# Performance work log

Hardware: AMD Instinct MI355X
Metric: run time of the kernel (lower is better)

## Reference

```python
import jax, jax.numpy as jnp
import numpy as np

N_EMBD = 768
N_HEAD = 12
HEAD_DIM = N_EMBD // N_HEAD  # 64


def setup_inputs() -> dict:
    key = jax.random.key(0)
    k1, k2, k3 = jax.random.split(key, 3)
    B, S = 4, 2048
    x = jax.random.normal(k1, (B, S, N_EMBD), dtype=jnp.float32)
    W_attn = jax.random.normal(k2, (N_EMBD, 3 * N_EMBD), dtype=jnp.float32) * 0.02
    b_attn = jax.random.normal(k3, (3 * N_EMBD,), dtype=jnp.float32) * 0.02
    return {"x": x, "W_attn": W_attn, "b_attn": b_attn}


def reference(x, W_attn, b_attn):
    B, S, E = x.shape
    H, D = N_HEAD, HEAD_DIM
    # fused QKV projection (torch Linear: x @ W^T + b; here W_attn stored as [E, 3E])
    qkv = x @ W_attn + b_attn  # [B, S, 3E]
    q, k, v = jnp.split(qkv, 3, axis=-1)
    q = q.reshape(B, S, H, D)
    k = k.reshape(B, S, H, D)
    v = v.reshape(B, S, H, D)
    scale = 1.0 / np.sqrt(D).astype(np.float32)
    scores = jnp.einsum('bqhd,bkhd->bhqk', q, k) * scale  # [B, H, S, S]
    causal = jnp.tril(jnp.ones((S, S), dtype=bool))
    # ReLU attention nonlinearity (no softmax); masked entries -> 0
    att = jnp.where(causal, jnp.maximum(scores, 0.0), 0.0)
    y = jnp.einsum('bhqk,bkhd->bqhd', att, v)  # [B, S, H, D]
    return y.reshape(B, S, E)
```

## Files before the change

### kernel.cpp

```cpp
#include <hip/hip_runtime.h>

typedef __attribute__((ext_vector_type(8))) short short8;
typedef __attribute__((ext_vector_type(4))) float floatx4;
typedef __attribute__((ext_vector_type(4))) unsigned int uint4v;

#define S_LEN 2048
#define NH 12
#define HD 64
#define EMB 768
#define E3 2304

#define MF(a, b, c) __builtin_amdgcn_mfma_f32_16x16x32_bf16(a, b, c, 0, 0, 0)

__device__ __forceinline__ unsigned short f2bf(float f) {
    unsigned int u = __builtin_bit_cast(unsigned int, f);
    u += 0x7FFFu + ((u >> 16) & 1u);
    return (unsigned short)(u >> 16);
}

__device__ __forceinline__ unsigned int pack2bf(float a, float b) {
#if __has_builtin(__builtin_amdgcn_cvt_pk_bf16_f32)
    typedef __attribute__((ext_vector_type(2))) short short2v;
    short2v r = __builtin_amdgcn_cvt_pk_bf16_f32(a, b);
    return __builtin_bit_cast(unsigned int, r);
#else
    return (unsigned int)f2bf(a) | ((unsigned int)f2bf(b) << 16);
#endif
}

__device__ __forceinline__ void pl32_swap(unsigned int& x, unsigned int& y) {
#if __has_builtin(__builtin_amdgcn_permlane32_swap)
    typedef __attribute__((ext_vector_type(2))) unsigned int uint2v_;
    uint2v_ r = __builtin_amdgcn_permlane32_swap(x, y, false, false);
    x = r[0]; y = r[1];
#else
    asm("v_permlane32_swap_b32 %0, %1" : "+v"(x), "+v"(y));
#endif
}
__device__ __forceinline__ void pl16_swap(unsigned int& x, unsigned int& y) {
#if __has_builtin(__builtin_amdgcn_permlane16_swap)
    typedef __attribute__((ext_vector_type(2))) unsigned int uint2v_;
    uint2v_ r = __builtin_amdgcn_permlane16_swap(x, y, false, false);
    x = r[0]; y = r[1];
#else
    asm("v_permlane16_swap_b32 %0, %1" : "+v"(x), "+v"(y));
#endif
}

__device__ __forceinline__ void gl_lds16(const void* g, void* l) {
    __builtin_amdgcn_global_load_lds(
        (const __attribute__((address_space(1))) unsigned int*)g,
        (__attribute__((address_space(3))) unsigned int*)l, 16, 0, 0);
}

__global__ __launch_bounds__(256) void conv_fused(const float* __restrict__ x,
                                                  ushort* __restrict__ xb,
                                                  const float* __restrict__ W,
                                                  ushort* __restrict__ Wt) {
    int tid = threadIdx.x;
    if (blockIdx.x < 6144) {
        int i = (blockIdx.x * 256 + tid) * 4;
        float4 f = *(const float4*)(x + i);
        ushort4 o;
        o.x = f2bf(f.x); o.y = f2bf(f.y); o.z = f2bf(f.z); o.w = f2bf(f.w);
        *(ushort4*)(xb + i) = o;
    } else {
        __shared__ float tile[32][33];
        int b2 = blockIdx.x - 6144;
        int n0 = (b2 % 72) * 32, k0 = (b2 / 72) * 32;
        int tx = tid & 31, ty = tid >> 5;
        for (int i = 0; i < 4; i++)
            tile[ty + i * 8][tx] = W[(size_t)(k0 + ty + i * 8) * E3 + n0 + tx];
        __syncthreads();
        for (int i = 0; i < 4; i++)
            Wt[(size_t)(n0 + ty + i * 8) * EMB + k0 + tx] = f2bf(tile[tx][ty + i * 8]);
    }
}

__global__ __launch_bounds__(512, 1) void qkv_gemm(const ushort* __restrict__ Xb,
                                                   const ushort* __restrict__ Wt,
                                                   const float* __restrict__ bias,
                                                   ushort* __restrict__ QKb,
                                                   ushort* __restrict__ Vt) {
    extern __shared__ char ldsb[];
    const int tid  = threadIdx.x;
    const int w = tid >> 6, lane = tid & 63;
    const int l15 = lane & 15, quad = lane >> 4;
    const int r8 = lane >> 3, cc = lane & 7;
    const int wm = w >> 1, wn = w & 1;
    const int m0 = blockIdx.x * 256, n0 = blockIdx.y * 128;

    floatx4 acc[4][4] = {};

    const char* agp = (const char*)Xb + (size_t)(m0 + w * 32 + r8) * 1536 + (cc ^ r8) * 16;
    const char* bgp = (const char*)Wt + (size_t)(n0 + w * 16 + r8) * 1536 + (cc ^ r8) * 16;
    const int adstB = w * 4096;
    const int bdstB = 32768 + w * 2048;

    const int aroB = (wm * 64 + l15) * 128;
    const int broB = 32768 + (wn * 64 + l15) * 128;
    const int swz0 = ((quad) ^ (l15 & 7)) * 16;
    const int swz1 = ((4 + quad) ^ (l15 & 7)) * 16;

    for (int i = 0; i < 4; i++) gl_lds16(agp + i * 12288, ldsb + adstB + i * 1024);
    for (int i = 0; i < 2; i++) gl_lds16(bgp + i * 12288, ldsb + bdstB + i * 1024);
    for (int i = 0; i < 4; i++) gl_lds16(agp + 128 + i * 12288, ldsb + 49152 + adstB + i * 1024);
    for (int i = 0; i < 2; i++) gl_lds16(bgp + 128 + i * 12288, ldsb + 49152 + bdstB + i * 1024);

#pragma unroll
    for (int t = 0; t < 12; ++t) {
        if (t < 11) asm volatile("s_waitcnt vmcnt(6)" ::: "memory");
        else        asm volatile("s_waitcnt vmcnt(0)" ::: "memory");
        __builtin_amdgcn_s_barrier();
        __builtin_amdgcn_sched_barrier(0);

        const char* base = ldsb + (t % 3) * 49152;
        char* sdst = ldsb + ((t + 2) % 3) * 49152;
        const int koff = (t + 2) * 128;
        const bool st = (t < 10);

        short8 af0, af1, bf0, bf1, bf2, bf3;

        af0 = *(const short8*)(base + aroB + 0 * 2048 + swz0);
        af1 = *(const short8*)(base + aroB + 1 * 2048 + swz0);
        bf0 = *(const short8*)(base + broB + 0 * 2048 + swz0);
        bf1 = *(const short8*)(base + broB + 1 * 2048 + swz0);
        bf2 = *(const short8*)(base + broB + 2 * 2048 + swz0);
        bf3 = *(const short8*)(base + broB + 3 * 2048 + swz0);
        if (st) { gl_lds16(agp + koff,         sdst + adstB);
                  gl_lds16(agp + koff + 12288, sdst + adstB + 1024); }
        __builtin_amdgcn_s_setprio(1);
        acc[0][0] = MF(af0, bf0, acc[0][0]); acc[0][1] = MF(af0, bf1, acc[0][1]);
        acc[0][2] = MF(af0, bf2, acc[0][2]); acc[0][3] = MF(af0, bf3, acc[0][3]);
        acc[1][0] = MF(af1, bf0, acc[1][0]); acc[1][1] = MF(af1, bf1, acc[1][1]);
        acc[1][2] = MF(af1, bf2, acc[1][2]); acc[1][3] = MF(af1, bf3, acc[1][3]);
        __builtin_amdgcn_s_setprio(0);
        __builtin_amdgcn_s_barrier();

        af0 = *(const short8*)(base + aroB + 2 * 2048 + swz0);
        af1 = *(const short8*)(base + aroB + 3 * 2048 + swz0);
        if (st) { gl_lds16(agp + koff + 2 * 12288, sdst + adstB + 2048);
                  gl_lds16(agp + koff + 3 * 12288, sdst + adstB + 3072); }
        __builtin_amdgcn_s_setprio(1);
        acc[2][0] = MF(af0, bf0, acc[2][0]); acc[2][1] = MF(af0, bf1, acc[2][1]);
        acc[2][2] = MF(af0, bf2, acc[2][2]); acc[2][3] = MF(af0, bf3, acc[2][3]);
        acc[3][0] = MF(af1, bf0, acc[3][0]); acc[3][1] = MF(af1, bf1, acc[3][1]);
        acc[3][2] = MF(af1, bf2, acc[3][2]); acc[3][3] = MF(af1, bf3, acc[3][3]);
        __builtin_amdgcn_s_setprio(0);
        __builtin_amdgcn_s_barrier();

        af0 = *(const short8*)(base + aroB + 0 * 2048 + swz1);
        af1 = *(const short8*)(base + aroB + 1 * 2048 + swz1);
        bf0 = *(const short8*)(base + broB + 0 * 2048 + swz1);
        bf1 = *(const short8*)(base + broB + 1 * 2048 + swz1);
        bf2 = *(const short8*)(base + broB + 2 * 2048 + swz1);
        bf3 = *(const short8*)(base + broB + 3 * 2048 + swz1);
        if (st) { gl_lds16(bgp + koff,         sdst + bdstB);
                  gl_lds16(bgp + koff + 12288, sdst + bdstB + 1024); }
        __builtin_amdgcn_s_setprio(1);
        acc[0][0] = MF(af0, bf0, acc[0][0]); acc[0][1] = MF(af0, bf1, acc[0][1]);
        acc[0][2] = MF(af0, bf2, acc[0][2]); acc[0][3] = MF(af0, bf3, acc[0][3]);
        acc[1][0] = MF(af1, bf0, acc[1][0]); acc[1][1] = MF(af1, bf1, acc[1][1]);
        acc[1][2] = MF(af1, bf2, acc[1][2]); acc[1][3] = MF(af1, bf3, acc[1][3]);
        __builtin_amdgcn_s_setprio(0);
        __builtin_amdgcn_s_barrier();

        af0 = *(const short8*)(base + aroB + 2 * 2048 + swz1);
        af1 = *(const short8*)(base + aroB + 3 * 2048 + swz1);
        __builtin_amdgcn_s_setprio(1);
        acc[2][0] = MF(af0, bf0, acc[2][0]); acc[2][1] = MF(af0, bf1, acc[2][1]);
        acc[2][2] = MF(af0, bf2, acc[2][2]); acc[2][3] = MF(af0, bf3, acc[2][3]);
        acc[3][0] = MF(af1, bf0, acc[3][0]); acc[3][1] = MF(af1, bf1, acc[3][1]);
        acc[3][2] = MF(af1, bf2, acc[3][2]); acc[3][3] = MF(af1, bf3, acc[3][3]);
        __builtin_amdgcn_s_setprio(0);
    }

    __syncthreads();
    ushort* epi = (ushort*)ldsb;
    int seg = n0 >= 1536 ? 2 : (n0 >= 768 ? 1 : 0);
    if (seg < 2) {
        float scale = (seg == 0) ? 0.125f : 1.0f;
        for (int ni = 0; ni < 4; ni++) {
            int nl = wn * 64 + ni * 16 + l15;
            float bv = bias[n0 + nl];
            for (int mi = 0; mi < 4; mi++)
                for (int r = 0; r < 4; r++) {
                    int ml = wm * 64 + mi * 16 + quad * 4 + r;
                    epi[ml * 132 + nl] = f2bf((acc[mi][ni][r] + bv) * scale);
                }
        }
        __syncthreads();
        int row = tid >> 1, h2 = tid & 1;
        size_t gm = (size_t)(m0 + row);
        for (int i = 0; i < 8; i++) {
            uint4 v = *(const uint4*)&epi[row * 132 + h2 * 64 + i * 8];
            *(uint4*)&QKb[gm * 1536 + n0 + h2 * 64 + i * 8] = v;
        }
    } else {
        for (int ni = 0; ni < 4; ni++) {
            int nl = wn * 64 + ni * 16 + l15;
            float bv = bias[n0 + nl];
            for (int mi = 0; mi < 4; mi++) {
                int ml = wm * 64 + mi * 16 + quad * 4;
                ushort4 p4;
                p4.x = f2bf(acc[mi][ni][0] + bv);
                p4.y = f2bf(acc[mi][ni][1] + bv);
                p4.z = f2bf(acc[mi][ni][2] + bv);
                p4.w = f2bf(acc[mi][ni][3] + bv);
                *(ushort4*)&epi[nl * 264 + ml] = p4;
            }
        }
        __syncthreads();
        int row = tid >> 2, q4 = tid & 3;
        int nn = n0 + row - 1536;
        int hh = nn >> 6, d = nn & 63;
        int bb = m0 >> 11, s0 = m0 & 2047;
        for (int i = 0; i < 8; i++) {
            uint4 v = *(const uint4*)&epi[row * 264 + q4 * 64 + i * 8];
            *(uint4*)&Vt[((size_t)(bb * NH + hh) * HD + d) * S_LEN + s0 + q4 * 64 + i * 8] = v;
        }
    }
}

__global__ __launch_bounds__(256) void attn(const ushort* __restrict__ QKb,
                                            const ushort* __restrict__ Vt,
                                            float* __restrict__ out) {
    __shared__ ushort lds[32768];
    char* ldsb = (char*)lds;
    int tid = threadIdx.x;
    int w = tid >> 6, lane = tid & 63;
    int l15 = lane & 15, quad = lane >> 4;
    int r8 = lane >> 3, cc = lane & 7;
    int rr = lane >> 4;

    int kfo[2];
    for (int ch = 0; ch < 2; ch++)
        kfo[ch] = l15 * 128 + ((ch * 4 + quad) ^ (l15 & 7)) * 16;
    int vfo2[4];
    for (int T = 0; T < 4; T++)
        vfo2[T] = 32768 + l15 * 256 + ((T * 4 + quad) ^ l15) * 16;
    int rhs[2] = { w * 32 + l15, w * 32 + 16 + l15 };
    int kgo = (w * 32 + r8) * 3072 + (cc ^ r8) * 16;
    int vgo[4];
    for (int i = 0; i < 4; i++)
        vgo[i] = (w * 16 + i * 4 + rr) * 4096 + (((lane & 15) ^ ((i * 4 + rr) & 15)) * 16);
    int kst = (w * 32) * 128;
    int vst = 32768 + (w * 16) * 256;

    int b = blockIdx.x;
    int nit, qts[2], bhs[2];
    if (b < 240)      { nit = 1; qts[0] = 15 - b / 48; bhs[0] = b % 48; qts[1] = 0; bhs[1] = 0; }
    else if (b < 480) { int j = b - 240; nit = 2; qts[0] = 10 - j / 48; bhs[0] = j % 48;
                        qts[1] = 1 + j / 48; bhs[1] = j % 48; }
    else              { int j = b - 480; nit = 2; qts[0] = 0; bhs[0] = 2 * j;
                        qts[1] = 0; bhs[1] = 2 * j + 1; }

    const char* kg[2]; const char* vg[2];
    for (int i = 0; i < 2; i++) {
        int bh = bhs[i], bg = bh / NH, h = bh % NH;
        kg[i] = (const char*)(QKb + (size_t)bg * S_LEN * 1536 + 768 + h * 64) + kgo;
        vg[i] = (const char*)(Vt + (size_t)bh * HD * S_LEN);
    }

    auto prefetch = [&](const char* kbase, const char* vbase, int dstP) {
        for (int i = 0; i < 4; i++)
            gl_lds16(kbase + i * 24576, ldsb + dstP * 16384 + kst + i * 1024);
        for (int i = 0; i < 4; i++)
            gl_lds16(vbase + vgo[i], ldsb + dstP * 16384 + vst + i * 1024);
    };

    int p = 0;
    prefetch(kg[0], vg[0], 0);
    for (int ii = 0; ii < nit; ii++) {
        int qt = qts[ii];
        int bh = bhs[ii], bg = bh / NH, h = bh % NH;
        const ushort* Qcol = QKb + (size_t)bg * S_LEN * 1536 + h * 64;
        short8 qf[2][2];
        for (int nq = 0; nq < 2; nq++)
            for (int ch = 0; ch < 2; ch++)
                qf[nq][ch] = *(const short8*)(Qcol +
                    (size_t)(qt * 128 + w * 32 + nq * 16 + l15) * 1536 + ch * 32 + quad * 8);

        floatx4 acco[2][4] = {};
        int nst = qt + 1;
        for (int st = 0; st < nst; st++) {
            __syncthreads();
            if (st + 1 < nst)
                prefetch(kg[ii] + (size_t)(st + 1) * 393216, vg[ii] + (st + 1) * 256, p ^ 1);
            else if (ii + 1 < nit)
                prefetch(kg[ii + 1], vg[ii + 1], p ^ 1);

            bool diag = (st == qt);
            const char* kb = ldsb + p * 16384;

            for (int jsub = 0; jsub < 2; jsub++) {
                floatx4 stc[4][2] = {};
                for (int ch = 0; ch < 2; ch++) {
                    short8 kf[4];
                    for (int mk = 0; mk < 4; mk++)
                        kf[mk] = *(const short8*)(kb + kfo[ch] + jsub * 8192 + mk * 2048);
                    for (int mk = 0; mk < 4; mk++)
                        for (int nq = 0; nq < 2; nq++)
                            stc[mk][nq] = __builtin_amdgcn_mfma_f32_16x16x32_bf16(
                                kf[mk], qf[nq][ch], stc[mk][nq], 0, 0, 0);
                }

                unsigned int pk[4][2][2];
                for (int mk = 0; mk < 4; mk++) {
                    for (int nq = 0; nq < 2; nq++) {
                        float e[4];
                        for (int r = 0; r < 4; r++)
                            e[r] = fmaxf(stc[mk][nq][r], 0.0f);
                        if (diag) {
                            int kl = jsub * 64 + mk * 16 + quad * 4;
                            for (int r = 0; r < 4; r++)
                                if (kl + r > rhs[nq]) e[r] = 0.0f;
                        }
                        pk[mk][nq][0] = pack2bf(e[0], e[1]);
                        pk[mk][nq][1] = pack2bf(e[2], e[3]);
                    }
                }

                for (int pr = 0; pr < 2; pr++) {
                    int T = jsub * 2 + pr;
                    short8 vf[4];
                    for (int ni = 0; ni < 4; ni++)
                        vf[ni] = *(const short8*)(kb + vfo2[T] + ni * 4096);
                    for (int mi = 0; mi < 2; mi++) {
                        unsigned int a0 = pk[2 * pr][mi][0], a1 = pk[2 * pr][mi][1];
                        unsigned int b0 = pk[2 * pr + 1][mi][0], b1 = pk[2 * pr + 1][mi][1];
                        pl32_swap(a0, b0);  pl32_swap(a1, b1);
                        pl16_swap(a0, b0);  pl16_swap(a1, b1);
                        short8 af = __builtin_bit_cast(short8, (uint4v){a0, a1, b0, b1});
                        for (int ni = 0; ni < 4; ni++)
                            acco[mi][ni] = __builtin_amdgcn_mfma_f32_16x16x32_bf16(
                                af, vf[ni], acco[mi][ni], 0, 0, 0);
                    }
                }
            }
            p ^= 1;
        }

        for (int mi = 0; mi < 2; mi++) {
            for (int ni = 0; ni < 4; ni++) {
                int d = ni * 16 + l15;
                for (int r = 0; r < 4; r++) {
                    int s = qt * 128 + w * 32 + mi * 16 + quad * 4 + r;
                    out[((size_t)bg * S_LEN + s) * EMB + h * 64 + d] = acco[mi][ni][r];
                }
            }
        }
    }
}

extern "C" void kernel_launch(void* const* d_in, const int* in_sizes, int n_in,
                              void* d_out, int out_size, void* d_ws, size_t ws_size,
                              hipStream_t stream) {
    const float* x    = (const float*)d_in[0];
    const float* W    = (const float*)d_in[1];
    const float* bias = (const float*)d_in[2];
    float* out = (float*)d_out;

    char* ws = (char*)d_ws;
    const size_t SZ_X  = (size_t)8192 * EMB * 2;
    const size_t SZ_W  = (size_t)E3 * EMB * 2;
    const size_t SZ_QK = (size_t)8192 * 1536 * 2;
    ushort* Xb  = (ushort*)(ws);
    ushort* Wt  = (ushort*)(ws + SZ_X);
    ushort* QKb = (ushort*)(ws + SZ_X + SZ_W);
    ushort* Vt  = (ushort*)(ws + SZ_X + SZ_W + SZ_QK);

    static bool attr_done = false;
    if (!attr_done) {
        hipFuncSetAttribute((const void*)qkv_gemm,
                            hipFuncAttributeMaxDynamicSharedMemorySize, 147456);
        attr_done = true;
    }

    conv_fused<<<dim3(6144 + 1728), dim3(256), 0, stream>>>(x, Xb, W, Wt);
    qkv_gemm<<<dim3(32, 18), dim3(512), 147456, stream>>>(Xb, Wt, bias, QKb, Vt);
    attn<<<dim3(504), dim3(256), 0, stream>>>(QKb, Vt, out);
}
```

Measured before the change: 186.5 us.

## Load V fragments directly from global, halve LDS, add occupancy and diagonal skip

V tiles are no longer staged through LDS. Each wave reads its V fragments straight from global memory into registers, which halves LDS use per block and lets launch_bounds request two blocks per CU. The change also staggers the jsub order across waves, skips the fully masked upper sub-block on the diagonal tile for the first two waves, and raises wave priority around the MFMA sections. The cost is uncoalesced global V loads whose latency is no longer hidden by async prefetch, along with tighter register pressure at the higher occupancy.

```diff
diff --git a/kernel.cpp b/kernel.cpp
--- a/kernel.cpp
+++ b/kernel.cpp
@@ -222,30 +222,23 @@
     }
 }
 
-__global__ __launch_bounds__(256) void attn(const ushort* __restrict__ QKb,
-                                            const ushort* __restrict__ Vt,
-                                            float* __restrict__ out) {
-    __shared__ ushort lds[32768];
+__global__ __launch_bounds__(256, 2) void attn(const ushort* __restrict__ QKb,
+                                               const ushort* __restrict__ Vt,
+                                               float* __restrict__ out) {
+    __shared__ ushort lds[16384];
     char* ldsb = (char*)lds;
     int tid = threadIdx.x;
     int w = tid >> 6, lane = tid & 63;
     int l15 = lane & 15, quad = lane >> 4;
     int r8 = lane >> 3, cc = lane & 7;
-    int rr = lane >> 4;
 
     int kfo[2];
     for (int ch = 0; ch < 2; ch++)
         kfo[ch] = l15 * 128 + ((ch * 4 + quad) ^ (l15 & 7)) * 16;
-    int vfo2[4];
-    for (int T = 0; T < 4; T++)
-        vfo2[T] = 32768 + l15 * 256 + ((T * 4 + quad) ^ l15) * 16;
     int rhs[2] = { w * 32 + l15, w * 32 + 16 + l15 };
     int kgo = (w * 32 + r8) * 3072 + (cc ^ r8) * 16;
-    int vgo[4];
-    for (int i = 0; i < 4; i++)
-        vgo[i] = (w * 16 + i * 4 + rr) * 4096 + (((lane & 15) ^ ((i * 4 + rr) & 15)) * 16);
     int kst = (w * 32) * 128;
-    int vst = 32768 + (w * 16) * 256;
+    const int vlo = l15 * S_LEN + quad * 8;
 
     int b = blockIdx.x;
     int nit, qts[2], bhs[2];
@@ -255,22 +248,20 @@
     else              { int j = b - 480; nit = 2; qts[0] = 0; bhs[0] = 2 * j;
                         qts[1] = 0; bhs[1] = 2 * j + 1; }
 
-    const char* kg[2]; const char* vg[2];
+    const char* kg[2]; const ushort* vb[2];
     for (int i = 0; i < 2; i++) {
         int bh = bhs[i], bg = bh / NH, h = bh % NH;
         kg[i] = (const char*)(QKb + (size_t)bg * S_LEN * 1536 + 768 + h * 64) + kgo;
-        vg[i] = (const char*)(Vt + (size_t)bh * HD * S_LEN);
-    }
-
-    auto prefetch = [&](const char* kbase, const char* vbase, int dstP) {
+        vb[i] = Vt + (size_t)bh * HD * S_LEN;
+    }
+
+    auto prefK = [&](const char* kbase, int dstP) {
         for (int i = 0; i < 4; i++)
             gl_lds16(kbase + i * 24576, ldsb + dstP * 16384 + kst + i * 1024);
-        for (int i = 0; i < 4; i++)
-            gl_lds16(vbase + vgo[i], ldsb + dstP * 16384 + vst + i * 1024);
     };
 
     int p = 0;
-    prefetch(kg[0], vg[0], 0);
+    prefK(kg[0], 0);
     for (int ii = 0; ii < nit; ii++) {
         int qt = qts[ii];
         int bh = bhs[ii], bg = bh / NH, h = bh % NH;
@@ -280,21 +271,34 @@
             for (int ch = 0; ch < 2; ch++)
                 qf[nq][ch] = *(const short8*)(Qcol +
                     (size_t)(qt * 128 + w * 32 + nq * 16 + l15) * 1536 + ch * 32 + quad * 8);
+        const ushort* vp[4];
+        for (int ni = 0; ni < 4; ni++)
+            vp[ni] = vb[ii] + (size_t)ni * 16 * S_LEN + vlo;
 
         floatx4 acco[2][4] = {};
         int nst = qt + 1;
         for (int st = 0; st < nst; st++) {
             __syncthreads();
             if (st + 1 < nst)
-                prefetch(kg[ii] + (size_t)(st + 1) * 393216, vg[ii] + (st + 1) * 256, p ^ 1);
+                prefK(kg[ii] + (size_t)(st + 1) * 393216, p ^ 1);
             else if (ii + 1 < nit)
-                prefetch(kg[ii + 1], vg[ii + 1], p ^ 1);
+                prefK(kg[ii + 1], p ^ 1);
 
             bool diag = (st == qt);
             const char* kb = ldsb + p * 16384;
-
-            for (int jsub = 0; jsub < 2; jsub++) {
+            int k0 = st * 128;
+
+            for (int js = 0; js < 2; js++) {
+                int jsub = js ^ (w & 1);
+                if (diag && w < 2 && jsub == 1) continue;
+
+                short8 vf[2][4];
+                for (int t2 = 0; t2 < 2; t2++)
+                    for (int ni = 0; ni < 4; ni++)
+                        vf[t2][ni] = *(const short8*)(vp[ni] + k0 + jsub * 64 + t2 * 32);
+
                 floatx4 stc[4][2] = {};
+                __builtin_amdgcn_s_setprio(1);
                 for (int ch = 0; ch < 2; ch++) {
                     short8 kf[4];
                     for (int mk = 0; mk < 4; mk++)
@@ -304,6 +308,7 @@
                             stc[mk][nq] = __builtin_amdgcn_mfma_f32_16x16x32_bf16(
                                 kf[mk], qf[nq][ch], stc[mk][nq], 0, 0, 0);
                 }
+                __builtin_amdgcn_s_setprio(0);
 
                 unsigned int pk[4][2][2];
                 for (int mk = 0; mk < 4; mk++) {
@@ -321,11 +326,8 @@
                     }
                 }
 
+                __builtin_amdgcn_s_setprio(1);
                 for (int pr = 0; pr < 2; pr++) {
-                    int T = jsub * 2 + pr;
-                    short8 vf[4];
-                    for (int ni = 0; ni < 4; ni++)
-                        vf[ni] = *(const short8*)(kb + vfo2[T] + ni * 4096);
                     for (int mi = 0; mi < 2; mi++) {
                         unsigned int a0 = pk[2 * pr][mi][0], a1 = pk[2 * pr][mi][1];
                         unsigned int b0 = pk[2 * pr + 1][mi][0], b1 = pk[2 * pr + 1][mi][1];
@@ -334,9 +336,10 @@
                         short8 af = __builtin_bit_cast(short8, (uint4v){a0, a1, b0, b1});
                         for (int ni = 0; ni < 4; ni++)
                             acco[mi][ni] = __builtin_amdgcn_mfma_f32_16x16x32_bf16(
-                                af, vf[ni], acco[mi][ni], 0, 0, 0);
+                                af, vf[pr][ni], acco[mi][ni], 0, 0, 0);
                     }
                 }
+                __builtin_amdgcn_s_setprio(0);
             }
             p ^= 1;
         }
```

Result: slower. 196.8 us (+5.6%).

## Process two adjacent query tiles per block sharing K/V tile loads

Applied to the files above, without the earlier changes.

The attention kernel now assigns each block a pair of adjacent 128-row query tiles for one (batch, head). Each K/V tile is streamed into LDS once and reused by both query tiles, replacing the previous 504-block load-balancing schedule with 384 blocks. Load imbalance remains because the tile pairs have different causal lengths. The change also adds s_setprio around the MFMA sections and a launch_bounds occupancy hint of 2, at the cost of more accumulator registers.

```diff
diff --git a/kernel.cpp b/kernel.cpp
--- a/kernel.cpp
+++ b/kernel.cpp
@@ -222,16 +222,15 @@
     }
 }
 
-__global__ __launch_bounds__(256) void attn(const ushort* __restrict__ QKb,
-                                            const ushort* __restrict__ Vt,
-                                            float* __restrict__ out) {
+__global__ __launch_bounds__(256, 2) void attn(const ushort* __restrict__ QKb,
+                                               const ushort* __restrict__ Vt,
+                                               float* __restrict__ out) {
     __shared__ ushort lds[32768];
     char* ldsb = (char*)lds;
     int tid = threadIdx.x;
     int w = tid >> 6, lane = tid & 63;
     int l15 = lane & 15, quad = lane >> 4;
     int r8 = lane >> 3, cc = lane & 7;
-    int rr = lane >> 4;
 
     int kfo[2];
     for (int ch = 0; ch < 2; ch++)
@@ -243,58 +242,60 @@
     int kgo = (w * 32 + r8) * 3072 + (cc ^ r8) * 16;
     int vgo[4];
     for (int i = 0; i < 4; i++)
-        vgo[i] = (w * 16 + i * 4 + rr) * 4096 + (((lane & 15) ^ ((i * 4 + rr) & 15)) * 16);
+        vgo[i] = (w * 16 + i * 4 + quad) * 4096 + ((l15 ^ ((i * 4 + quad) & 15)) * 16);
     int kst = (w * 32) * 128;
     int vst = 32768 + (w * 16) * 256;
 
     int b = blockIdx.x;
-    int nit, qts[2], bhs[2];
-    if (b < 240)      { nit = 1; qts[0] = 15 - b / 48; bhs[0] = b % 48; qts[1] = 0; bhs[1] = 0; }
-    else if (b < 480) { int j = b - 240; nit = 2; qts[0] = 10 - j / 48; bhs[0] = j % 48;
-                        qts[1] = 1 + j / 48; bhs[1] = j % 48; }
-    else              { int j = b - 480; nit = 2; qts[0] = 0; bhs[0] = 2 * j;
-                        qts[1] = 0; bhs[1] = 2 * j + 1; }
-
-    const char* kg[2]; const char* vg[2];
-    for (int i = 0; i < 2; i++) {
-        int bh = bhs[i], bg = bh / NH, h = bh % NH;
-        kg[i] = (const char*)(QKb + (size_t)bg * S_LEN * 1536 + 768 + h * 64) + kgo;
-        vg[i] = (const char*)(Vt + (size_t)bh * HD * S_LEN);
-    }
-
-    auto prefetch = [&](const char* kbase, const char* vbase, int dstP) {
+    int j = 7 - b / 48, bh = b % 48;
+    int qts2[2] = { 2 * j, 2 * j + 1 };
+    int bg = bh / NH, h = bh % NH;
+    const char* kg = (const char*)(QKb + (size_t)bg * S_LEN * 1536 + 768 + h * 64) + kgo;
+    const char* vgb = (const char*)(Vt + (size_t)bh * HD * S_LEN);
+
+    auto prefetch = [&](int st, int dstP) {
+        const char* kbase = kg + (size_t)st * 393216;
+        const char* vbase = vgb + st * 256;
         for (int i = 0; i < 4; i++)
             gl_lds16(kbase + i * 24576, ldsb + dstP * 16384 + kst + i * 1024);
         for (int i = 0; i < 4; i++)
             gl_lds16(vbase + vgo[i], ldsb + dstP * 16384 + vst + i * 1024);
     };
 
-    int p = 0;
-    prefetch(kg[0], vg[0], 0);
-    for (int ii = 0; ii < nit; ii++) {
-        int qt = qts[ii];
-        int bh = bhs[ii], bg = bh / NH, h = bh % NH;
-        const ushort* Qcol = QKb + (size_t)bg * S_LEN * 1536 + h * 64;
-        short8 qf[2][2];
+    const ushort* Qcol = QKb + (size_t)bg * S_LEN * 1536 + h * 64;
+    short8 qf[2][2][2];
+    for (int tq = 0; tq < 2; tq++)
         for (int nq = 0; nq < 2; nq++)
             for (int ch = 0; ch < 2; ch++)
-                qf[nq][ch] = *(const short8*)(Qcol +
-                    (size_t)(qt * 128 + w * 32 + nq * 16 + l15) * 1536 + ch * 32 + quad * 8);
-
-        floatx4 acco[2][4] = {};
-        int nst = qt + 1;
-        for (int st = 0; st < nst; st++) {
-            __syncthreads();
-            if (st + 1 < nst)
-                prefetch(kg[ii] + (size_t)(st + 1) * 393216, vg[ii] + (st + 1) * 256, p ^ 1);
-            else if (ii + 1 < nit)
-                prefetch(kg[ii + 1], vg[ii + 1], p ^ 1);
-
-            bool diag = (st == qt);
-            const char* kb = ldsb + p * 16384;
-
-            for (int jsub = 0; jsub < 2; jsub++) {
+                qf[tq][nq][ch] = *(const short8*)(Qcol +
+                    (size_t)(qts2[tq] * 128 + w * 32 + nq * 16 + l15) * 1536 + ch * 32 + quad * 8);
+
+    floatx4 acco[2][2][4] = {};
+    int nst = qts2[1] + 1;
+    int p = 0;
+    prefetch(0, 0);
+    for (int st = 0; st < nst; st++) {
+        __syncthreads();
+        if (st + 1 < nst) prefetch(st + 1, p ^ 1);
+
+        const char* kb = ldsb + p * 16384;
+
+#pragma unroll
+        for (int jsub = 0; jsub < 2; jsub++) {
+            short8 vf[2][4];
+            for (int pr = 0; pr < 2; pr++) {
+                int T = jsub * 2 + pr;
+                for (int ni = 0; ni < 4; ni++)
+                    vf[pr][ni] = *(const short8*)(kb + vfo2[T] + ni * 4096);
+            }
+
+#pragma unroll
+            for (int tq = 0; tq < 2; tq++) {
+                if (st > qts2[tq]) continue;
+                bool diag = (st == qts2[tq]);
+
                 floatx4 stc[4][2] = {};
+                __builtin_amdgcn_s_setprio(1);
                 for (int ch = 0; ch < 2; ch++) {
                     short8 kf[4];
                     for (int mk = 0; mk < 4; mk++)
@@ -302,8 +303,9 @@
                     for (int mk = 0; mk < 4; mk++)
                         for (int nq = 0; nq < 2; nq++)
                             stc[mk][nq] = __builtin_amdgcn_mfma_f32_16x16x32_bf16(
-                                kf[mk], qf[nq][ch], stc[mk][nq], 0, 0, 0);
-                }
+                                kf[mk], qf[tq][nq][ch], stc[mk][nq], 0, 0, 0);
+                }
+                __builtin_amdgcn_s_setprio(0);
 
                 unsigned int pk[4][2][2];
                 for (int mk = 0; mk < 4; mk++) {
@@ -321,11 +323,8 @@
                     }
                 }
 
+                __builtin_amdgcn_s_setprio(1);
                 for (int pr = 0; pr < 2; pr++) {
-                    int T = jsub * 2 + pr;
-                    short8 vf[4];
-                    for (int ni = 0; ni < 4; ni++)
-                        vf[ni] = *(const short8*)(kb + vfo2[T] + ni * 4096);
                     for (int mi = 0; mi < 2; mi++) {
                         unsigned int a0 = pk[2 * pr][mi][0], a1 = pk[2 * pr][mi][1];
                         unsigned int b0 = pk[2 * pr + 1][mi][0], b1 = pk[2 * pr + 1][mi][1];
@@ -333,20 +332,23 @@
                         pl16_swap(a0, b0);  pl16_swap(a1, b1);
                         short8 af = __builtin_bit_cast(short8, (uint4v){a0, a1, b0, b1});
                         for (int ni = 0; ni < 4; ni++)
-                            acco[mi][ni] = __builtin_amdgcn_mfma_f32_16x16x32_bf16(
-                                af, vf[ni], acco[mi][ni], 0, 0, 0);
+                            acco[tq][mi][ni] = __builtin_amdgcn_mfma_f32_16x16x32_bf16(
+                                af, vf[pr][ni], acco[tq][mi][ni], 0, 0, 0);
                     }
                 }
+                __builtin_amdgcn_s_setprio(0);
             }
-            p ^= 1;
-        }
-
+        }
+        p ^= 1;
+    }
+
+    for (int tq = 0; tq < 2; tq++) {
         for (int mi = 0; mi < 2; mi++) {
             for (int ni = 0; ni < 4; ni++) {
                 int d = ni * 16 + l15;
                 for (int r = 0; r < 4; r++) {
-                    int s = qt * 128 + w * 32 + mi * 16 + quad * 4 + r;
-                    out[((size_t)bg * S_LEN + s) * EMB + h * 64 + d] = acco[mi][ni][r];
+                    int s = qts2[tq] * 128 + w * 32 + mi * 16 + quad * 4 + r;
+                    out[((size_t)bg * S_LEN + s) * EMB + h * 64 + d] = acco[tq][mi][ni][r];
                 }
             }
         }
@@ -379,5 +381,5 @@
 
     conv_fused<<<dim3(6144 + 1728), dim3(256), 0, stream>>>(x, Xb, W, Wt);
     qkv_gemm<<<dim3(32, 18), dim3(512), 147456, stream>>>(Xb, Wt, bias, QKb, Vt);
-    attn<<<dim3(504), dim3(256), 0, stream>>>(QKb, Vt, out);
-}
+    attn<<<dim3(384), dim3(256), 0, stream>>>(QKb, Vt, out);
+}
```

Measured after the change: 189.8 us. No clear change (+1.8%).

## Shrink attention tiles to 64 queries and 64 keys per block, drop paired scheduling

Applied to the files above, without the earlier changes.

The attention kernel now uses 128-thread blocks handling a 64-row query tile with 64-key stages, launching 1536 blocks ordered longest-first instead of 504 blocks that paired short and long tiles. LDS usage halves and launch bounds allow multiple blocks per CU, aiming at better load balance and occupancy across the causal triangle. The trade-off is that each K/V stage is reused by fewer queries, which means more global/LDS traffic per FLOP and more barriers per unit of work.

```diff
diff --git a/kernel.cpp b/kernel.cpp
--- a/kernel.cpp
+++ b/kernel.cpp
@@ -222,132 +222,115 @@
     }
 }
 
-__global__ __launch_bounds__(256) void attn(const ushort* __restrict__ QKb,
-                                            const ushort* __restrict__ Vt,
-                                            float* __restrict__ out) {
-    __shared__ ushort lds[32768];
+__global__ __launch_bounds__(128, 2) void attn(const ushort* __restrict__ QKb,
+                                               const ushort* __restrict__ Vt,
+                                               float* __restrict__ out) {
+    __shared__ ushort lds[16384];
     char* ldsb = (char*)lds;
     int tid = threadIdx.x;
     int w = tid >> 6, lane = tid & 63;
     int l15 = lane & 15, quad = lane >> 4;
     int r8 = lane >> 3, cc = lane & 7;
-    int rr = lane >> 4;
 
     int kfo[2];
     for (int ch = 0; ch < 2; ch++)
         kfo[ch] = l15 * 128 + ((ch * 4 + quad) ^ (l15 & 7)) * 16;
-    int vfo2[4];
-    for (int T = 0; T < 4; T++)
-        vfo2[T] = 32768 + l15 * 256 + ((T * 4 + quad) ^ l15) * 16;
+    int vfo[2];
+    for (int T = 0; T < 2; T++)
+        vfo[T] = 16384 + l15 * 128 + ((T * 4 + quad) ^ (l15 & 7)) * 16;
     int rhs[2] = { w * 32 + l15, w * 32 + 16 + l15 };
     int kgo = (w * 32 + r8) * 3072 + (cc ^ r8) * 16;
     int vgo[4];
     for (int i = 0; i < 4; i++)
-        vgo[i] = (w * 16 + i * 4 + rr) * 4096 + (((lane & 15) ^ ((i * 4 + rr) & 15)) * 16);
+        vgo[i] = (w * 32 + i * 8 + r8) * 4096 + (cc ^ r8) * 16;
     int kst = (w * 32) * 128;
-    int vst = 32768 + (w * 16) * 256;
+    int vst = 16384 + (w * 32) * 128;
 
     int b = blockIdx.x;
-    int nit, qts[2], bhs[2];
-    if (b < 240)      { nit = 1; qts[0] = 15 - b / 48; bhs[0] = b % 48; qts[1] = 0; bhs[1] = 0; }
-    else if (b < 480) { int j = b - 240; nit = 2; qts[0] = 10 - j / 48; bhs[0] = j % 48;
-                        qts[1] = 1 + j / 48; bhs[1] = j % 48; }
-    else              { int j = b - 480; nit = 2; qts[0] = 0; bhs[0] = 2 * j;
-                        qts[1] = 0; bhs[1] = 2 * j + 1; }
-
-    const char* kg[2]; const char* vg[2];
-    for (int i = 0; i < 2; i++) {
-        int bh = bhs[i], bg = bh / NH, h = bh % NH;
-        kg[i] = (const char*)(QKb + (size_t)bg * S_LEN * 1536 + 768 + h * 64) + kgo;
-        vg[i] = (const char*)(Vt + (size_t)bh * HD * S_LEN);
-    }
-
-    auto prefetch = [&](const char* kbase, const char* vbase, int dstP) {
+    int qs = 31 - b / 48, bh = b % 48;
+    int bg = bh / NH, h = bh % NH;
+
+    const char* kg = (const char*)(QKb + (size_t)bg * S_LEN * 1536 + 768 + h * 64) + kgo;
+    const char* vgb = (const char*)(Vt + (size_t)bh * HD * S_LEN);
+
+    auto prefetch = [&](int st, int dstP) {
+        const char* kbase = kg + (size_t)st * 196608;
+        const char* vbase = vgb + st * 128;
         for (int i = 0; i < 4; i++)
-            gl_lds16(kbase + i * 24576, ldsb + dstP * 16384 + kst + i * 1024);
+            gl_lds16(kbase + i * 24576, ldsb + dstP * 8192 + kst + i * 1024);
         for (int i = 0; i < 4; i++)
-            gl_lds16(vbase + vgo[i], ldsb + dstP * 16384 + vst + i * 1024);
+            gl_lds16(vbase + vgo[i], ldsb + dstP * 8192 + vst + i * 1024);
     };
 
+    const ushort* Qcol = QKb + (size_t)bg * S_LEN * 1536 + h * 64;
+    short8 qf[2][2];
+    for (int nq = 0; nq < 2; nq++)
+        for (int ch = 0; ch < 2; ch++)
+            qf[nq][ch] = *(const short8*)(Qcol +
+                (size_t)(qs * 64 + w * 32 + nq * 16 + l15) * 1536 + ch * 32 + quad * 8);
+
+    floatx4 acco[2][4] = {};
     int p = 0;
-    prefetch(kg[0], vg[0], 0);
-    for (int ii = 0; ii < nit; ii++) {
-        int qt = qts[ii];
-        int bh = bhs[ii], bg = bh / NH, h = bh % NH;
-        const ushort* Qcol = QKb + (size_t)bg * S_LEN * 1536 + h * 64;
-        short8 qf[2][2];
-        for (int nq = 0; nq < 2; nq++)
-            for (int ch = 0; ch < 2; ch++)
-                qf[nq][ch] = *(const short8*)(Qcol +
-                    (size_t)(qt * 128 + w * 32 + nq * 16 + l15) * 1536 + ch * 32 + quad * 8);
-
-        floatx4 acco[2][4] = {};
-        int nst = qt + 1;
-        for (int st = 0; st < nst; st++) {
-            __syncthreads();
-            if (st + 1 < nst)
-                prefetch(kg[ii] + (size_t)(st + 1) * 393216, vg[ii] + (st + 1) * 256, p ^ 1);
-            else if (ii + 1 < nit)
-                prefetch(kg[ii + 1], vg[ii + 1], p ^ 1);
-
-            bool diag = (st == qt);
-            const char* kb = ldsb + p * 16384;
-
-            for (int jsub = 0; jsub < 2; jsub++) {
-                floatx4 stc[4][2] = {};
-                for (int ch = 0; ch < 2; ch++) {
-                    short8 kf[4];
-                    for (int mk = 0; mk < 4; mk++)
-                        kf[mk] = *(const short8*)(kb + kfo[ch] + jsub * 8192 + mk * 2048);
-                    for (int mk = 0; mk < 4; mk++)
-                        for (int nq = 0; nq < 2; nq++)
-                            stc[mk][nq] = __builtin_amdgcn_mfma_f32_16x16x32_bf16(
-                                kf[mk], qf[nq][ch], stc[mk][nq], 0, 0, 0);
+    prefetch(0, 0);
+    int nst = qs + 1;
+    for (int st = 0; st < nst; st++) {
+        __syncthreads();
+        if (st + 1 < nst) prefetch(st + 1, p ^ 1);
+
+        bool diag = (st == qs);
+        const char* kb = ldsb + p * 8192;
+
+        floatx4 stc[4][2] = {};
+        for (int ch = 0; ch < 2; ch++) {
+            short8 kf[4];
+            for (int mk = 0; mk < 4; mk++)
+                kf[mk] = *(const short8*)(kb + kfo[ch] + mk * 2048);
+            for (int mk = 0; mk < 4; mk++)
+                for (int nq = 0; nq < 2; nq++)
+                    stc[mk][nq] = __builtin_amdgcn_mfma_f32_16x16x32_bf16(
+                        kf[mk], qf[nq][ch], stc[mk][nq], 0, 0, 0);
+        }
+
+        unsigned int pk[4][2][2];
+        for (int mk = 0; mk < 4; mk++) {
+            for (int nq = 0; nq < 2; nq++) {
+                float e[4];
+                for (int r = 0; r < 4; r++)
+                    e[r] = fmaxf(stc[mk][nq][r], 0.0f);
+                if (diag) {
+                    int kl = mk * 16 + quad * 4;
+                    for (int r = 0; r < 4; r++)
+                        if (kl + r > rhs[nq]) e[r] = 0.0f;
                 }
-
-                unsigned int pk[4][2][2];
-                for (int mk = 0; mk < 4; mk++) {
-                    for (int nq = 0; nq < 2; nq++) {
-                        float e[4];
-                        for (int r = 0; r < 4; r++)
-                            e[r] = fmaxf(stc[mk][nq][r], 0.0f);
-                        if (diag) {
-                            int kl = jsub * 64 + mk * 16 + quad * 4;
-                            for (int r = 0; r < 4; r++)
-                                if (kl + r > rhs[nq]) e[r] = 0.0f;
-                        }
-                        pk[mk][nq][0] = pack2bf(e[0], e[1]);
-                        pk[mk][nq][1] = pack2bf(e[2], e[3]);
-                    }
-                }
-
-                for (int pr = 0; pr < 2; pr++) {
-                    int T = jsub * 2 + pr;
-                    short8 vf[4];
-                    for (int ni = 0; ni < 4; ni++)
-                        vf[ni] = *(const short8*)(kb + vfo2[T] + ni * 4096);
-                    for (int mi = 0; mi < 2; mi++) {
-                        unsigned int a0 = pk[2 * pr][mi][0], a1 = pk[2 * pr][mi][1];
-                        unsigned int b0 = pk[2 * pr + 1][mi][0], b1 = pk[2 * pr + 1][mi][1];
-                        pl32_swap(a0, b0);  pl32_swap(a1, b1);
-                        pl16_swap(a0, b0);  pl16_swap(a1, b1);
-                        short8 af = __builtin_bit_cast(short8, (uint4v){a0, a1, b0, b1});
-                        for (int ni = 0; ni < 4; ni++)
-                            acco[mi][ni] = __builtin_amdgcn_mfma_f32_16x16x32_bf16(
-                                af, vf[ni], acco[mi][ni], 0, 0, 0);
-                    }
-                }
+                pk[mk][nq][0] = pack2bf(e[0], e[1]);
+                pk[mk][nq][1] = pack2bf(e[2], e[3]);
             }
-            p ^= 1;
-        }
-
-        for (int mi = 0; mi < 2; mi++) {
-            for (int ni = 0; ni < 4; ni++) {
-                int d = ni * 16 + l15;
-                for (int r = 0; r < 4; r++) {
-                    int s = qt * 128 + w * 32 + mi * 16 + quad * 4 + r;
-                    out[((size_t)bg * S_LEN + s) * EMB + h * 64 + d] = acco[mi][ni][r];
-                }
+        }
+
+        for (int pr = 0; pr < 2; pr++) {
+            short8 vf[4];
+            for (int ni = 0; ni < 4; ni++)
+                vf[ni] = *(const short8*)(kb + vfo[pr] + ni * 2048);
+            for (int mi = 0; mi < 2; mi++) {
+                unsigned int a0 = pk[2 * pr][mi][0], a1 = pk[2 * pr][mi][1];
+                unsigned int b0 = pk[2 * pr + 1][mi][0], b1 = pk[2 * pr + 1][mi][1];
+                pl32_swap(a0, b0);  pl32_swap(a1, b1);
+                pl16_swap(a0, b0);  pl16_swap(a1, b1);
+                short8 af = __builtin_bit_cast(short8, (uint4v){a0, a1, b0, b1});
+                for (int ni = 0; ni < 4; ni++)
+                    acco[mi][ni] = __builtin_amdgcn_mfma_f32_16x16x32_bf16(
+                        af, vf[ni], acco[mi][ni], 0, 0, 0);
+            }
+        }
+        p ^= 1;
+    }
+
+    for (int mi = 0; mi < 2; mi++) {
+        for (int ni = 0; ni < 4; ni++) {
+            int d = ni * 16 + l15;
+            for (int r = 0; r < 4; r++) {
+                int s = qs * 64 + w * 32 + mi * 16 + quad * 4 + r;
+                out[((size_t)bg * S_LEN + s) * EMB + h * 64 + d] = acco[mi][ni][r];
             }
         }
     }
@@ -379,5 +362,5 @@
 
     conv_fused<<<dim3(6144 + 1728), dim3(256), 0, stream>>>(x, Xb, W, Wt);
     qkv_gemm<<<dim3(32, 18), dim3(512), 147456, stream>>>(Xb, Wt, bias, QKb, Vt);
-    attn<<<dim3(504), dim3(256), 0, stream>>>(QKb, Vt, out);
-}
+    attn<<<dim3(1536), dim3(128), 0, stream>>>(QKb, Vt, out);
+}
```

New measurement: 186.0 us. No clear change (-0.2%).
